# Performance work log

Hardware: AMD Instinct MI355X
Metric: run time of the kernel (lower is better)

Reference implementation:

```python
import jax, jax.numpy as jnp
import numpy as np

N = 100000
E = 1600000
IN_C = 128
OUT_C = 8
HEADS = 8
EDGE_DIM = 4
ACTUAL_OUT = OUT_C * HEADS  # 64, concat=True
BN_EPS = 1e-5
NEG_SLOPE = 0.2  # PyG GATConv default leaky_relu slope


def setup_inputs() -> dict:
    key = jax.random.key(0)
    ks = jax.random.split(key, 12)
    s = lambda fan_in: 1.0 / np.sqrt(fan_in)
    return {
        "x": jax.random.normal(ks[0], (N, IN_C), jnp.float32),
        "edge_index": jax.random.randint(ks[1], (2, E), 0, N, jnp.int64),
        "edge_attr": jax.random.normal(ks[2], (E, EDGE_DIM), jnp.float32),
        # GATConv params
        "W": jax.random.normal(ks[3], (IN_C, HEADS * OUT_C), jnp.float32) * s(IN_C),
        "att_src": jax.random.normal(ks[4], (HEADS, OUT_C), jnp.float32) * s(OUT_C),
        "att_dst": jax.random.normal(ks[5], (HEADS, OUT_C), jnp.float32) * s(OUT_C),
        "W_edge": jax.random.normal(ks[6], (EDGE_DIM, HEADS * OUT_C), jnp.float32) * s(EDGE_DIM),
        "att_edge": jax.random.normal(ks[7], (HEADS, OUT_C), jnp.float32) * s(OUT_C),
        "bias": jnp.zeros((HEADS * OUT_C,), jnp.float32),
        # BatchNorm params
        "bn_w": jnp.ones((ACTUAL_OUT,), jnp.float32),
        "bn_b": jnp.zeros((ACTUAL_OUT,), jnp.float32),
        # residual Linear (in_channels != heads*out_channels)
        "res_W": jax.random.normal(ks[8], (IN_C, ACTUAL_OUT), jnp.float32) * s(IN_C),
        "res_b": jnp.zeros((ACTUAL_OUT,), jnp.float32),
    }


def reference(x, edge_index, edge_attr, W, att_src, att_dst, W_edge, att_edge,
              bias, bn_w, bn_b, res_W, res_b):
    src, dst = edge_index[0], edge_index[1]
    n = x.shape[0]

    # --- GATConv (PyG semantics, eval mode: dropout is identity) ---
    h = (x @ W).reshape(n, HEADS, OUT_C)                       # [N,H,C]
    a_src = jnp.einsum('nhc,hc->nh', h, att_src)               # [N,H]
    a_dst = jnp.einsum('nhc,hc->nh', h, att_dst)               # [N,H]
    he = (edge_attr @ W_edge).reshape(-1, HEADS, OUT_C)        # [E,H,C]
    a_edge = jnp.einsum('ehc,hc->eh', he, att_edge)            # [E,H]

    logits = jax.nn.leaky_relu(a_src[src] + a_dst[dst] + a_edge, NEG_SLOPE)  # [E,H]
    # segment softmax over edges grouped by destination node
    m = jax.ops.segment_max(logits, dst, num_segments=n)       # [N,H]
    m = jnp.where(jnp.isfinite(m), m, 0.0)
    num = jnp.exp(logits - jax.lax.stop_gradient(m)[dst])      # [E,H]
    denom = jax.ops.segment_sum(num, dst, num_segments=n)      # [N,H]
    alpha = num / (denom[dst] + 1e-16)                         # [E,H]

    msg = alpha[:, :, None] * h[src]                           # [E,H,C]
    out = jax.ops.segment_sum(msg, dst, num_segments=n)        # [N,H,C]
    out = out.reshape(n, HEADS * OUT_C) + bias                 # concat heads

    # --- BatchNorm (training-mode batch stats, biased variance) ---
    mean = out.mean(axis=0)
    var = out.var(axis=0)
    out = (out - mean) * jax.lax.rsqrt(var + BN_EPS) * bn_w + bn_b

    # --- ELU, (dropout=identity in eval), residual ---
    out = jax.nn.elu(out)
    identity = x @ res_W + res_b
    return out + identity
```

## Files before the change

kernel.cpp:

```cpp
#include <hip/hip_runtime.h>
#include <hip/hip_bf16.h>

#define N_NODES 100000
#define N_EDGES 1600000

typedef unsigned short ushort_t;
typedef __attribute__((ext_vector_type(4))) float f32x4;
typedef __attribute__((ext_vector_type(8))) short bf16x8v;

__device__ __forceinline__ float rlane(float v, int l) {
    return __int_as_float(__builtin_amdgcn_readlane(__float_as_int(v), l));
}
__device__ __forceinline__ ushort_t f2bf(float f) {
    unsigned u = __float_as_uint(f);
    u += 0x7FFFu + ((u >> 16) & 1u);
    return (ushort_t)(u >> 16);
}
__device__ __forceinline__ float bf2f(ushort_t b) {
    return __uint_as_float((unsigned)b << 16);
}
__device__ __forceinline__ void atomic_pk_add_bf16(ushort_t* addr, unsigned packed) {
    asm volatile("global_atomic_pk_add_bf16 %0, %1, off sc1"
                 :: "v"(addr), "v"(packed) : "memory");
}

__global__ __launch_bounds__(256) void k1_mfma(
    const float* __restrict__ x, const float* __restrict__ W,
    const float* __restrict__ resW, const float* __restrict__ att_src,
    const float* __restrict__ att_dst, const float* __restrict__ res_b,
    ushort_t* __restrict__ h, float* __restrict__ ident,
    float* __restrict__ a_src, float* __restrict__ a_dst)
{
    const int lane = threadIdx.x & 63;
    const int col = lane & 15;
    const int kg  = lane >> 4;

    bf16x8v bfrag[4][8];
    #pragma unroll
    for (int ks = 0; ks < 4; ++ks) {
        #pragma unroll
        for (int fc = 0; fc < 8; ++fc) {
            const int j = (fc & 3) * 16 + col;
            const float* src = (fc < 4) ? (W + j) : (resW + j);
            bf16x8v b;
            #pragma unroll
            for (int i = 0; i < 8; ++i) {
                const int k = ks * 32 + kg * 8 + i;
                b[i] = (short)f2bf(src[k * 64]);
            }
            bfrag[ks][fc] = b;
        }
    }
    float atts[4], attd[4], rb[4];
    #pragma unroll
    for (int fc = 0; fc < 4; ++fc) {
        atts[fc] = att_src[fc * 16 + col];
        attd[fc] = att_dst[fc * 16 + col];
        rb[fc]   = res_b[fc * 16 + col];
    }

    const int wid = blockIdx.x * 4 + (threadIdx.x >> 6);
    const int nw = gridDim.x * 4;
    for (int tile = wid; tile < 3125; tile += nw) {
        const int row0 = tile * 32;
        f32x4 acc[2][8];
        #pragma unroll
        for (int rt = 0; rt < 2; ++rt)
            #pragma unroll
            for (int fc = 0; fc < 8; ++fc)
                acc[rt][fc] = (f32x4){0.f, 0.f, 0.f, 0.f};

        #pragma unroll
        for (int ks = 0; ks < 4; ++ks) {
            bf16x8v afrag[2];
            #pragma unroll
            for (int rt = 0; rt < 2; ++rt) {
                const float* xr = x + (size_t)(row0 + rt * 16 + col) * 128 + ks * 32 + kg * 8;
                const float4 lo = *reinterpret_cast<const float4*>(xr);
                const float4 hi = *reinterpret_cast<const float4*>(xr + 4);
                bf16x8v a;
                a[0] = (short)f2bf(lo.x); a[1] = (short)f2bf(lo.y);
                a[2] = (short)f2bf(lo.z); a[3] = (short)f2bf(lo.w);
                a[4] = (short)f2bf(hi.x); a[5] = (short)f2bf(hi.y);
                a[6] = (short)f2bf(hi.z); a[7] = (short)f2bf(hi.w);
                afrag[rt] = a;
            }
            #pragma unroll
            for (int fc = 0; fc < 8; ++fc) {
                acc[0][fc] = __builtin_amdgcn_mfma_f32_16x16x32_bf16(
                    afrag[0], bfrag[ks][fc], acc[0][fc], 0, 0, 0);
                acc[1][fc] = __builtin_amdgcn_mfma_f32_16x16x32_bf16(
                    afrag[1], bfrag[ks][fc], acc[1][fc], 0, 0, 0);
            }
        }

        #pragma unroll
        for (int rt = 0; rt < 2; ++rt) {
            #pragma unroll
            for (int fc = 0; fc < 8; ++fc) {
                #pragma unroll
                for (int r = 0; r < 4; ++r) {
                    const int row = row0 + rt * 16 + kg * 4 + r;
                    const float val = acc[rt][fc][r];
                    if (fc < 4) {
                        h[(size_t)row * 64 + fc * 16 + col] = f2bf(val);
                        float ps = val * atts[fc];
                        float pd = val * attd[fc];
                        ps += __shfl_xor(ps, 1); ps += __shfl_xor(ps, 2); ps += __shfl_xor(ps, 4);
                        pd += __shfl_xor(pd, 1); pd += __shfl_xor(pd, 2); pd += __shfl_xor(pd, 4);
                        if ((lane & 7) == 0) {
                            const int hd = fc * 2 + (col >> 3);
                            a_src[row * 8 + hd] = ps;
                            a_dst[row * 8 + hd] = pd;
                        }
                    } else {
                        ident[(size_t)row * 64 + (fc - 4) * 16 + col] = val + rb[fc - 4];
                    }
                }
            }
        }
    }
}

__global__ __launch_bounds__(256) void k2_edge(
    const int* __restrict__ ei, const float* __restrict__ ea,
    const ushort_t* __restrict__ h, const float* __restrict__ a_src,
    const float* __restrict__ a_dst, const float* __restrict__ W_edge,
    const float* __restrict__ att_edge,
    float* __restrict__ denom, ushort_t* __restrict__ out_raw)
{
    const int lane = threadIdx.x & 63;
    const int hd = lane >> 3;
    float ae0 = 0.f, ae1 = 0.f, ae2 = 0.f, ae3 = 0.f;
    #pragma unroll
    for (int c2 = 0; c2 < 8; ++c2) {
        const float a = att_edge[hd * 8 + c2];
        ae0 = fmaf(W_edge[0 * 64 + hd * 8 + c2], a, ae0);
        ae1 = fmaf(W_edge[1 * 64 + hd * 8 + c2], a, ae1);
        ae2 = fmaf(W_edge[2 * 64 + hd * 8 + c2], a, ae2);
        ae3 = fmaf(W_edge[3 * 64 + hd * 8 + c2], a, ae3);
    }

    const int gwave = blockIdx.x * 4 + (threadIdx.x >> 6);
    const int nwave = gridDim.x * 4;
    for (int base = gwave * 64; base < N_EDGES; base += nwave * 64) {
        const int vsrc = ei[base + lane];
        const int vdst = ei[N_EDGES + base + lane];
        const float4 vea = *reinterpret_cast<const float4*>(ea + (size_t)(base + lane) * 4);
        for (int g = 0; g < 64; g += 8) {
            int s[8], d[8];
            float e0[8], e1[8], e2[8], e3[8];
            #pragma unroll
            for (int j = 0; j < 8; ++j) {
                s[j] = __builtin_amdgcn_readlane(vsrc, g + j);
                d[j] = __builtin_amdgcn_readlane(vdst, g + j);
                e0[j] = rlane(vea.x, g + j);
                e1[j] = rlane(vea.y, g + j);
                e2[j] = rlane(vea.z, g + j);
                e3[j] = rlane(vea.w, g + j);
            }
            float hv[8], as8[8], ad8[8];
            #pragma unroll
            for (int j = 0; j < 8; ++j) {
                hv[j]  = bf2f(h[(size_t)s[j] * 64 + lane]);
                as8[j] = a_src[s[j] * 8 + hd];
                ad8[j] = a_dst[d[j] * 8 + hd];
            }
            #pragma unroll
            for (int j = 0; j < 8; ++j) {
                float logit = as8[j] + ad8[j]
                            + e0[j] * ae0 + e1[j] * ae1 + e2[j] * ae2 + e3[j] * ae3;
                logit = logit > 0.f ? logit : 0.2f * logit;
                const float num = __expf(logit);
                const float v = num * hv[j];
                const float vn = __shfl_xor(v, 1);
                if ((lane & 1) == 0) {
                    const unsigned packed = (unsigned)f2bf(v) | ((unsigned)f2bf(vn) << 16);
                    atomic_pk_add_bf16(out_raw + (size_t)d[j] * 64 + lane, packed);
                }
                if ((lane & 7) == 0) atomicAdd(&denom[d[j] * 8 + hd], num);
            }
        }
    }
    asm volatile("s_waitcnt vmcnt(0)" ::: "memory");
}

__global__ __launch_bounds__(256) void k3_stats(
    const ushort_t* __restrict__ out_raw, const float* __restrict__ denom,
    const float* __restrict__ bias,
    float* __restrict__ bn_acc )
{
    const int tid = threadIdx.x;
    const int c = tid & 63;
    const float b = bias[c];
    float s1 = 0.f, s2 = 0.f;
    const int stride = gridDim.x * 4;
    for (int n = blockIdx.x * 4 + (tid >> 6); n < N_NODES; n += stride) {
        const float v = bf2f(out_raw[(size_t)n * 64 + c])
                        / (denom[n * 8 + (c >> 3)] + 1e-16f) + b;
        s1 += v; s2 += v * v;
    }
    __shared__ float r1[256], r2[256];
    r1[tid] = s1; r2[tid] = s2;
    __syncthreads();
    if (tid < 64) {
        s1 = r1[tid] + r1[tid + 64] + r1[tid + 128] + r1[tid + 192];
        s2 = r2[tid] + r2[tid + 64] + r2[tid + 128] + r2[tid + 192];
        atomicAdd(&bn_acc[c], s1);
        atomicAdd(&bn_acc[64 + c], s2);
    }
}

__global__ __launch_bounds__(256) void k4_final(
    float* __restrict__ out, const ushort_t* __restrict__ out_raw,
    const float* __restrict__ denom, const float* __restrict__ bias,
    const float* __restrict__ bn_acc, const float* __restrict__ bn_w,
    const float* __restrict__ bn_b)
{
    const int tid = threadIdx.x;
    const int c = tid & 63;
    const float b = bias[c];
    const float inv_n = 1.0f / (float)N_NODES;
    const float mean = bn_acc[c] * inv_n;
    const float var = bn_acc[64 + c] * inv_n - mean * mean;
    const float sc = bn_w[c] * rsqrtf(var + 1e-5f);
    const float sh = bn_b[c] - mean * sc;
    const int stride = gridDim.x * 4;
    for (int n = blockIdx.x * 4 + (tid >> 6); n < N_NODES; n += stride) {
        float v = bf2f(out_raw[(size_t)n * 64 + c])
                  / (denom[n * 8 + (c >> 3)] + 1e-16f) + b;
        v = v * sc + sh;
        v = v > 0.f ? v : __expf(v) - 1.f;
        out[(size_t)n * 64 + c] = v + out[(size_t)n * 64 + c];
    }
}

extern "C" void kernel_launch(void* const* d_in, const int* in_sizes, int n_in,
                              void* d_out, int out_size, void* d_ws, size_t ws_size,
                              hipStream_t stream) {
    const float* x        = (const float*)d_in[0];
    const int*   ei       = (const int*)  d_in[1];
    const float* ea       = (const float*)d_in[2];
    const float* W        = (const float*)d_in[3];
    const float* att_src  = (const float*)d_in[4];
    const float* att_dst  = (const float*)d_in[5];
    const float* W_edge   = (const float*)d_in[6];
    const float* att_edge = (const float*)d_in[7];
    const float* bias     = (const float*)d_in[8];
    const float* bn_w     = (const float*)d_in[9];
    const float* bn_b     = (const float*)d_in[10];
    const float* res_W    = (const float*)d_in[11];
    const float* res_b    = (const float*)d_in[12];

    char* ws = (char*)d_ws;
    size_t off = 0;
    ushort_t* h   = (ushort_t*)(ws + off); off += (size_t)N_NODES * 64 * 2;
    float* a_src  = (float*)(ws + off); off += (size_t)N_NODES * 8 * 4;
    float* a_dst  = (float*)(ws + off); off += (size_t)N_NODES * 8 * 4;
    char*  zstart = ws + off;
    float* denom  = (float*)(ws + off); off += (size_t)N_NODES * 8 * 4;
    ushort_t* o_raw = (ushort_t*)(ws + off); off += (size_t)N_NODES * 64 * 2;
    float* bn_acc = (float*)(ws + off); off += 128 * 4;
    size_t zbytes = (size_t)((ws + off) - zstart);

    float* ident = (float*)d_out;

    (void)hipMemsetAsync(zstart, 0, zbytes, stream);
    k1_mfma<<<512, 256, 0, stream>>>(
        x, W, res_W, att_src, att_dst, res_b, h, ident, a_src, a_dst);
    k2_edge<<<6250, 256, 0, stream>>>(ei, ea, h, a_src, a_dst, W_edge, att_edge,
                                      denom, o_raw);
    k3_stats<<<2048, 256, 0, stream>>>(o_raw, denom, bias, bn_acc);
    k4_final<<<2048, 256, 0, stream>>>((float*)d_out, o_raw, denom, bias,
                                       bn_acc, bn_w, bn_b);
}
```

Baseline: 484.3 us.

## Build destination-sorted CSR per call and replace atomic scatter with per-node gather

Computes a degree histogram, prefix scan and counting-sort scatter of edges by destination, then processes each destination node in one wave, accumulating softmax numerator and denominator in registers. This removes the per-edge bf16 packed atomics and denom atomics, and fuses normalization, bias and BN statistic accumulation into the gather kernel, dropping the separate stats pass. It adds three preprocessing kernels including a serial single-block scan, and quantizes edge attributes to bf16 in the sorted copy.

```diff
diff --git a/kernel.cpp b/kernel.cpp
--- a/kernel.cpp
+++ b/kernel.cpp
@@ -11,17 +11,13 @@
 __device__ __forceinline__ float rlane(float v, int l) {
     return __int_as_float(__builtin_amdgcn_readlane(__float_as_int(v), l));
 }
-__device__ __forceinline__ ushort_t f2bf(float f) {
+__device__ __forceinline__ unsigned f2bf(float f) {
     unsigned u = __float_as_uint(f);
     u += 0x7FFFu + ((u >> 16) & 1u);
-    return (ushort_t)(u >> 16);
-}
-__device__ __forceinline__ float bf2f(ushort_t b) {
-    return __uint_as_float((unsigned)b << 16);
-}
-__device__ __forceinline__ void atomic_pk_add_bf16(ushort_t* addr, unsigned packed) {
-    asm volatile("global_atomic_pk_add_bf16 %0, %1, off sc1"
-                 :: "v"(addr), "v"(packed) : "memory");
+    return u >> 16;
+}
+__device__ __forceinline__ float bf2f(unsigned b) {
+    return __uint_as_float((b & 0xFFFFu) << 16);
 }
 
 __global__ __launch_bounds__(256) void k1_mfma(
@@ -103,7 +99,7 @@
                     const int row = row0 + rt * 16 + kg * 4 + r;
                     const float val = acc[rt][fc][r];
                     if (fc < 4) {
-                        h[(size_t)row * 64 + fc * 16 + col] = f2bf(val);
+                        h[(size_t)row * 64 + fc * 16 + col] = (ushort_t)f2bf(val);
                         float ps = val * atts[fc];
                         float pd = val * attd[fc];
                         ps += __shfl_xor(ps, 1); ps += __shfl_xor(ps, 2); ps += __shfl_xor(ps, 4);
@@ -122,14 +118,64 @@
     }
 }
 
-__global__ __launch_bounds__(256) void k2_edge(
+__global__ __launch_bounds__(256) void k2a_hist(const int* __restrict__ ei,
+                                                int* __restrict__ deg) {
+    for (int e = blockIdx.x * 256 + threadIdx.x; e < N_EDGES; e += gridDim.x * 256)
+        atomicAdd(&deg[ei[N_EDGES + e]], 1);
+}
+
+__global__ __launch_bounds__(1024) void k2b_scan(const int* __restrict__ deg,
+                                                 int* __restrict__ roff,
+                                                 int* __restrict__ wcur) {
+    __shared__ int part[1024];
+    __shared__ int pre[1024];
+    __shared__ int stot;
+    const int tid = threadIdx.x;
+    const int start = tid * 98;
+    const int end = (start + 98 < N_NODES) ? start + 98 : N_NODES;
+    int local = 0;
+    for (int i = start; i < end; ++i) local += deg[i];
+    part[tid] = local;
+    __syncthreads();
+    if (tid == 0) {
+        int run = 0;
+        for (int t = 0; t < 1024; ++t) { pre[t] = run; run += part[t]; }
+        stot = run;
+    }
+    __syncthreads();
+    int run = pre[tid];
+    for (int i = start; i < end; ++i) {
+        roff[i] = run; wcur[i] = run; run += deg[i];
+    }
+    if (tid == 0) roff[N_NODES] = stot;
+}
+
+__global__ __launch_bounds__(256) void k2c_scatter(
     const int* __restrict__ ei, const float* __restrict__ ea,
-    const ushort_t* __restrict__ h, const float* __restrict__ a_src,
-    const float* __restrict__ a_dst, const float* __restrict__ W_edge,
-    const float* __restrict__ att_edge,
-    float* __restrict__ denom, ushort_t* __restrict__ out_raw)
+    int* __restrict__ wcur, int* __restrict__ es, uint2* __restrict__ epk) {
+    for (int e = blockIdx.x * 256 + threadIdx.x; e < N_EDGES; e += gridDim.x * 256) {
+        const int s = ei[e];
+        const int d = ei[N_EDGES + e];
+        const float4 v = *reinterpret_cast<const float4*>(ea + (size_t)e * 4);
+        const int pos = atomicAdd(&wcur[d], 1);
+        es[pos] = s;
+        uint2 p;
+        p.x = f2bf(v.x) | (f2bf(v.y) << 16);
+        p.y = f2bf(v.z) | (f2bf(v.w) << 16);
+        epk[pos] = p;
+    }
+}
+
+__global__ __launch_bounds__(256) void k2d_accum(
+    const int* __restrict__ roff, const int* __restrict__ es,
+    const uint2* __restrict__ epk, const ushort_t* __restrict__ h,
+    const float* __restrict__ a_src, const float* __restrict__ a_dst,
+    const float* __restrict__ W_edge, const float* __restrict__ att_edge,
+    const float* __restrict__ bias,
+    ushort_t* __restrict__ out16, float* __restrict__ bn_acc)
 {
-    const int lane = threadIdx.x & 63;
+    const int tid = threadIdx.x;
+    const int lane = tid & 63;
     const int hd = lane >> 3;
     float ae0 = 0.f, ae1 = 0.f, ae2 = 0.f, ae3 = 0.f;
     #pragma unroll
@@ -140,86 +186,83 @@
         ae2 = fmaf(W_edge[2 * 64 + hd * 8 + c2], a, ae2);
         ae3 = fmaf(W_edge[3 * 64 + hd * 8 + c2], a, ae3);
     }
-
-    const int gwave = blockIdx.x * 4 + (threadIdx.x >> 6);
-    const int nwave = gridDim.x * 4;
-    for (int base = gwave * 64; base < N_EDGES; base += nwave * 64) {
-        const int vsrc = ei[base + lane];
-        const int vdst = ei[N_EDGES + base + lane];
-        const float4 vea = *reinterpret_cast<const float4*>(ea + (size_t)(base + lane) * 4);
-        for (int g = 0; g < 64; g += 8) {
-            int s[8], d[8];
-            float e0[8], e1[8], e2[8], e3[8];
+    const float bia = bias[lane];
+    float s1 = 0.f, s2 = 0.f;
+
+    const int gw = blockIdx.x * 4 + (tid >> 6);
+    const int nw = gridDim.x * 4;
+    for (int d = gw; d < N_NODES; d += nw) {
+        const int row = roff[d];
+        const int dg = roff[d + 1] - row;
+        const float adv = a_dst[d * 8 + hd];
+        float acc = 0.f, den = 0.f;
+
+        int vs = 0; uint2 vp; vp.x = 0; vp.y = 0;
+        if (lane < dg) { vs = es[row + lane]; vp = epk[row + lane]; }
+        const int m = dg < 64 ? dg : 64;
+
+        for (int g = 0; g < m; g += 8) {
+            int sj[8]; float dj[8];
             #pragma unroll
             for (int j = 0; j < 8; ++j) {
-                s[j] = __builtin_amdgcn_readlane(vsrc, g + j);
-                d[j] = __builtin_amdgcn_readlane(vdst, g + j);
-                e0[j] = rlane(vea.x, g + j);
-                e1[j] = rlane(vea.y, g + j);
-                e2[j] = rlane(vea.z, g + j);
-                e3[j] = rlane(vea.w, g + j);
-            }
-            float hv[8], as8[8], ad8[8];
+                int idx = g + j; const bool ok = idx < m; idx = ok ? idx : 0;
+                sj[j] = __builtin_amdgcn_readlane(vs, idx);
+                const unsigned px = (unsigned)__builtin_amdgcn_readlane((int)vp.x, idx);
+                const unsigned py = (unsigned)__builtin_amdgcn_readlane((int)vp.y, idx);
+                float dd = bf2f(px) * ae0 + bf2f(px >> 16) * ae1
+                         + bf2f(py) * ae2 + bf2f(py >> 16) * ae3;
+                dj[j] = ok ? dd : -1e30f;
+            }
+            float as8[8], hv[8];
             #pragma unroll
             for (int j = 0; j < 8; ++j) {
-                hv[j]  = bf2f(h[(size_t)s[j] * 64 + lane]);
-                as8[j] = a_src[s[j] * 8 + hd];
-                ad8[j] = a_dst[d[j] * 8 + hd];
+                as8[j] = a_src[sj[j] * 8 + hd];
+                hv[j]  = bf2f(h[(size_t)sj[j] * 64 + lane]);
             }
             #pragma unroll
             for (int j = 0; j < 8; ++j) {
-                float logit = as8[j] + ad8[j]
-                            + e0[j] * ae0 + e1[j] * ae1 + e2[j] * ae2 + e3[j] * ae3;
+                float logit = as8[j] + adv + dj[j];
                 logit = logit > 0.f ? logit : 0.2f * logit;
                 const float num = __expf(logit);
-                const float v = num * hv[j];
-                const float vn = __shfl_xor(v, 1);
-                if ((lane & 1) == 0) {
-                    const unsigned packed = (unsigned)f2bf(v) | ((unsigned)f2bf(vn) << 16);
-                    atomic_pk_add_bf16(out_raw + (size_t)d[j] * 64 + lane, packed);
-                }
-                if ((lane & 7) == 0) atomicAdd(&denom[d[j] * 8 + hd], num);
-            }
-        }
-    }
-    asm volatile("s_waitcnt vmcnt(0)" ::: "memory");
-}
-
-__global__ __launch_bounds__(256) void k3_stats(
-    const ushort_t* __restrict__ out_raw, const float* __restrict__ denom,
-    const float* __restrict__ bias,
-    float* __restrict__ bn_acc )
-{
-    const int tid = threadIdx.x;
-    const int c = tid & 63;
-    const float b = bias[c];
-    float s1 = 0.f, s2 = 0.f;
-    const int stride = gridDim.x * 4;
-    for (int n = blockIdx.x * 4 + (tid >> 6); n < N_NODES; n += stride) {
-        const float v = bf2f(out_raw[(size_t)n * 64 + c])
-                        / (denom[n * 8 + (c >> 3)] + 1e-16f) + b;
+                den += num;
+                acc = fmaf(num, hv[j], acc);
+            }
+        }
+        for (int i = 64; i < dg; ++i) {
+            const int s = es[row + i];
+            const uint2 p = epk[row + i];
+            float logit = a_src[s * 8 + hd] + adv
+                        + bf2f(p.x) * ae0 + bf2f(p.x >> 16) * ae1
+                        + bf2f(p.y) * ae2 + bf2f(p.y >> 16) * ae3;
+            logit = logit > 0.f ? logit : 0.2f * logit;
+            const float num = __expf(logit);
+            den += num;
+            acc = fmaf(num, bf2f(h[(size_t)s * 64 + lane]), acc);
+        }
+
+        const float v = acc / (den + 1e-16f) + bia;
+        out16[(size_t)d * 64 + lane] = (ushort_t)f2bf(v);
         s1 += v; s2 += v * v;
     }
+
     __shared__ float r1[256], r2[256];
     r1[tid] = s1; r2[tid] = s2;
     __syncthreads();
     if (tid < 64) {
         s1 = r1[tid] + r1[tid + 64] + r1[tid + 128] + r1[tid + 192];
         s2 = r2[tid] + r2[tid + 64] + r2[tid + 128] + r2[tid + 192];
-        atomicAdd(&bn_acc[c], s1);
-        atomicAdd(&bn_acc[64 + c], s2);
+        atomicAdd(&bn_acc[tid], s1);
+        atomicAdd(&bn_acc[64 + tid], s2);
     }
 }
 
 __global__ __launch_bounds__(256) void k4_final(
-    float* __restrict__ out, const ushort_t* __restrict__ out_raw,
-    const float* __restrict__ denom, const float* __restrict__ bias,
+    float* __restrict__ out, const ushort_t* __restrict__ out16,
     const float* __restrict__ bn_acc, const float* __restrict__ bn_w,
     const float* __restrict__ bn_b)
 {
     const int tid = threadIdx.x;
     const int c = tid & 63;
-    const float b = bias[c];
     const float inv_n = 1.0f / (float)N_NODES;
     const float mean = bn_acc[c] * inv_n;
     const float var = bn_acc[64 + c] * inv_n - mean * mean;
@@ -227,8 +270,7 @@
     const float sh = bn_b[c] - mean * sc;
     const int stride = gridDim.x * 4;
     for (int n = blockIdx.x * 4 + (tid >> 6); n < N_NODES; n += stride) {
-        float v = bf2f(out_raw[(size_t)n * 64 + c])
-                  / (denom[n * 8 + (c >> 3)] + 1e-16f) + b;
+        float v = bf2f(out16[(size_t)n * 64 + c]);
         v = v * sc + sh;
         v = v > 0.f ? v : __expf(v) - 1.f;
         out[(size_t)n * 64 + c] = v + out[(size_t)n * 64 + c];
@@ -254,13 +296,17 @@
 
     char* ws = (char*)d_ws;
     size_t off = 0;
-    ushort_t* h   = (ushort_t*)(ws + off); off += (size_t)N_NODES * 64 * 2;
-    float* a_src  = (float*)(ws + off); off += (size_t)N_NODES * 8 * 4;
-    float* a_dst  = (float*)(ws + off); off += (size_t)N_NODES * 8 * 4;
-    char*  zstart = ws + off;
-    float* denom  = (float*)(ws + off); off += (size_t)N_NODES * 8 * 4;
-    ushort_t* o_raw = (ushort_t*)(ws + off); off += (size_t)N_NODES * 64 * 2;
-    float* bn_acc = (float*)(ws + off); off += 128 * 4;
+    ushort_t* h     = (ushort_t*)(ws + off); off += (size_t)N_NODES * 64 * 2;
+    float* a_src    = (float*)(ws + off); off += (size_t)N_NODES * 8 * 4;
+    float* a_dst    = (float*)(ws + off); off += (size_t)N_NODES * 8 * 4;
+    ushort_t* out16 = (ushort_t*)(ws + off); off += (size_t)N_NODES * 64 * 2;
+    int* es         = (int*)(ws + off); off += (size_t)N_EDGES * 4;
+    uint2* epk      = (uint2*)(ws + off); off += (size_t)N_EDGES * 8;
+    int* roff       = (int*)(ws + off); off += (size_t)(N_NODES + 1) * 4;
+    char* zstart = ws + off;
+    int* deg        = (int*)(ws + off); off += (size_t)N_NODES * 4;
+    int* wcur       = (int*)(ws + off); off += (size_t)N_NODES * 4;
+    float* bn_acc   = (float*)(ws + off); off += 128 * 4;
     size_t zbytes = (size_t)((ws + off) - zstart);
 
     float* ident = (float*)d_out;
@@ -268,9 +314,10 @@
     (void)hipMemsetAsync(zstart, 0, zbytes, stream);
     k1_mfma<<<512, 256, 0, stream>>>(
         x, W, res_W, att_src, att_dst, res_b, h, ident, a_src, a_dst);
-    k2_edge<<<6250, 256, 0, stream>>>(ei, ea, h, a_src, a_dst, W_edge, att_edge,
-                                      denom, o_raw);
-    k3_stats<<<2048, 256, 0, stream>>>(o_raw, denom, bias, bn_acc);
-    k4_final<<<2048, 256, 0, stream>>>((float*)d_out, o_raw, denom, bias,
-                                       bn_acc, bn_w, bn_b);
-}
+    k2a_hist<<<2048, 256, 0, stream>>>(ei, deg);
+    k2b_scan<<<1, 1024, 0, stream>>>(deg, roff, wcur);
+    k2c_scatter<<<2048, 256, 0, stream>>>(ei, ea, wcur, es, epk);
+    k2d_accum<<<2048, 256, 0, stream>>>(roff, es, epk, h, a_src, a_dst,
+                                        W_edge, att_edge, bias, out16, bn_acc);
+    k4_final<<<2048, 256, 0, stream>>>((float*)d_out, out16, bn_acc, bn_w, bn_b);
+}
```

After: 715.9 us. 1.48x slower.
